# Kernel optimization log

Hardware: AMD Instinct MI355X
Metric: run time of the kernel (lower is better)

The kernel has to match this reference:

```python
import jax, jax.numpy as jnp
import numpy as np

D_MODEL = 1024
NUM_HEADS = 16
D_K = D_MODEL // NUM_HEADS


def setup_inputs() -> dict:
    key = jax.random.key(0)
    k1, k2, k3, k4 = jax.random.split(key, 4)
    x = jax.random.normal(k1, (2, 2048, D_MODEL), dtype=jnp.float32)
    # qkv_proj: Linear(d_model, 3*d_model, bias=False); stored as [in, out] for x @ W
    W_qkv = jax.random.normal(k2, (D_MODEL, 3 * D_MODEL), dtype=jnp.float32) * (1.0 / np.sqrt(D_MODEL))
    W_out = jax.random.normal(k3, (D_MODEL, D_MODEL), dtype=jnp.float32) * (1.0 / np.sqrt(D_MODEL))
    b_out = jax.random.normal(k4, (D_MODEL,), dtype=jnp.float32) * 0.01
    return {"x": x, "W_qkv": W_qkv, "W_out": W_out, "b_out": b_out}


def reference(x, W_qkv, W_out, b_out):
    B, N, C = x.shape
    scale = 1.0 / np.sqrt(D_K)
    qkv = (x @ W_qkv).reshape(B, N, 3, NUM_HEADS, D_K)
    qkv = jnp.transpose(qkv, (2, 0, 3, 1, 4))  # [3, B, H, N, d_k]
    q, k, v = qkv[0], qkv[1], qkv[2]
    scores = jnp.einsum("bhqd,bhkd->bhqk", q, k) * scale  # [B,H,N,N]
    attn = jax.nn.softmax(scores, axis=-1)
    out = jnp.einsum("bhqk,bhkd->bhqd", attn, v)  # [B,H,N,d_k]
    out = jnp.transpose(out, (0, 2, 1, 3)).reshape(B, N, C)
    return out @ W_out + b_out
```

## Files before the change

### kernel.cpp

```cpp
#include <hip/hip_runtime.h>
#include <cstdint>

typedef __bf16 bf16_t;
typedef __bf16 bf16x8 __attribute__((ext_vector_type(8)));
typedef float  f32x4  __attribute__((ext_vector_type(4)));
typedef uint32_t u32x4 __attribute__((ext_vector_type(4)));

#define MFMA16(a,b,c) __builtin_amdgcn_mfma_f32_16x16x32_bf16((a),(b),(c),0,0,0)

__device__ __forceinline__ void gload_lds16(const bf16_t* g, bf16_t* l) {
  __builtin_amdgcn_global_load_lds(
      (const __attribute__((address_space(1))) unsigned int*)g,
      (__attribute__((address_space(3))) unsigned int*)l,
      16, 0, 0);
}

__device__ __forceinline__ uint32_t cvt_pk_bf16(float lo, float hi) {
  uint32_t r;
  asm("v_cvt_pk_bf16_f32 %0, %1, %2" : "=v"(r) : "v"(lo), "v"(hi));
  return r;
}

__global__ void k_conv_x(const float* __restrict__ x, bf16_t* __restrict__ xb) {
  int i = blockIdx.x * blockDim.x + threadIdx.x;
  const float4* p = reinterpret_cast<const float4*>(x) + (size_t)i * 2;
  float4 a = p[0], b = p[1];
  bf16x8 v;
  v[0]=(bf16_t)a.x; v[1]=(bf16_t)a.y; v[2]=(bf16_t)a.z; v[3]=(bf16_t)a.w;
  v[4]=(bf16_t)b.x; v[5]=(bf16_t)b.y; v[6]=(bf16_t)b.z; v[7]=(bf16_t)b.w;
  *reinterpret_cast<bf16x8*>(xb + (size_t)i * 8) = v;
}

__global__ void k_transpose_w(const float* __restrict__ W, bf16_t* __restrict__ WT,
                              int K, int N) {
  __shared__ float tile[32][33];
  int n0 = blockIdx.x * 32, k0 = blockIdx.y * 32;
  int c = threadIdx.x & 31, r8 = threadIdx.x >> 5;
#pragma unroll
  for (int rr = 0; rr < 4; rr++) {
    int r = r8 + rr * 8;
    tile[r][c] = W[(size_t)(k0 + r) * N + n0 + c];
  }
  __syncthreads();
#pragma unroll
  for (int rr = 0; rr < 4; rr++) {
    int r = r8 + rr * 8;
    WT[(size_t)(n0 + r) * K + k0 + c] = (bf16_t)tile[c][r];
  }
}

__global__ void k_vtrans(const bf16_t* __restrict__ V, bf16_t* __restrict__ VT) {
  __shared__ bf16_t t[64 * 72];
  int bi = blockIdx.x;
  int head = bi >> 5, kt = bi & 31;
  int tid = threadIdx.x;
  const bf16_t* src = V + (size_t)head * 131072 + (size_t)kt * 64 * 64;
#pragma unroll
  for (int j = 0; j < 2; j++) {
    int q = tid + 256 * j;
    int key = q >> 3, part = q & 7;
    bf16x8 v = *reinterpret_cast<const bf16x8*>(src + key * 64 + part * 8);
    *reinterpret_cast<bf16x8*>(&t[key * 72 + part * 8]) = v;
  }
  __syncthreads();
  bf16_t* dst = VT + (size_t)head * 131072 + kt * 64;
#pragma unroll
  for (int j = 0; j < 2; j++) {
    int q = tid + 256 * j;
    int dv = q >> 3, part = q & 7;
    bf16x8 v;
#pragma unroll
    for (int e = 0; e < 8; e++) v[e] = t[(part * 8 + e) * 72 + dv];
    *reinterpret_cast<bf16x8*>(dst + (size_t)dv * 2048 + part * 8) = v;
  }
}

template<int EPI, int MT>
__global__ __launch_bounds__(256, 2) void k_gemm(
    const bf16_t* __restrict__ A, const bf16_t* __restrict__ BT, int Klen,
    bf16_t* __restrict__ Qo, bf16_t* __restrict__ Ko, bf16_t* __restrict__ Vo,
    const float* __restrict__ bias, float* __restrict__ Out, int Nout) {
  constexpr int WM = MT / 2;
  constexpr int MF = WM / 16;
  __shared__ bf16_t As[2][MT * 32];
  __shared__ bf16_t Bs[2][4096];
  int tid = threadIdx.x, lane = tid & 63, wid = tid >> 6;
  int row0 = blockIdx.x * MT, col0 = blockIdx.y * 128;
  int wr = wid >> 1, wc = wid & 1;
  int g = lane >> 4, li = lane & 15;

  f32x4 acc[MF][4] = {};

  auto stage = [&](int buf, int kt) {
    int k0 = kt * 32;
#pragma unroll
    for (int j = 0; j < MT / 64; j++) {
      int q = tid + 256 * j;
      int r = q >> 2, part = q & 3;
      gload_lds16(A + (size_t)(row0 + r) * Klen + k0 + part * 8,
                  &As[buf][q * 8]);
    }
#pragma unroll
    for (int j = 0; j < 2; j++) {
      int q = tid + 256 * j;
      int r = q >> 2, part = q & 3;
      gload_lds16(BT + (size_t)(col0 + r) * Klen + k0 + part * 8,
                  &Bs[buf][q * 8]);
    }
  };

  int nk = Klen >> 5;
  stage(0, 0);
  for (int kt = 0; kt < nk; kt++) {
    __syncthreads();
    if (kt + 1 < nk) stage((kt + 1) & 1, kt + 1);
    int buf = kt & 1;
    int kl = g * 8;
    bf16x8 a[MF], b[4];
#pragma unroll
    for (int m = 0; m < MF; m++)
      a[m] = *reinterpret_cast<const bf16x8*>(&As[buf][(wr * WM + m * 16 + li) * 32 + kl]);
#pragma unroll
    for (int n = 0; n < 4; n++)
      b[n] = *reinterpret_cast<const bf16x8*>(&Bs[buf][(wc * 64 + n * 16 + li) * 32 + kl]);
#pragma unroll
    for (int m = 0; m < MF; m++)
#pragma unroll
      for (int n = 0; n < 4; n++)
        acc[m][n] = MFMA16(a[m], b[n], acc[m][n]);
  }

#pragma unroll
  for (int m = 0; m < MF; m++) {
    int rg = row0 + wr * WM + m * 16 + g * 4;
#pragma unroll
    for (int n = 0; n < 4; n++) {
      int cg = col0 + wc * 64 + n * 16 + li;
#pragma unroll
      for (int i = 0; i < 4; i++) {
        float v = acc[m][n][i];
        int row = rg + i;
        if constexpr (EPI == 0) {
          int t = cg >> 10, h = (cg >> 6) & 15, dk = cg & 63;
          int b2 = row >> 11, nn = row & 2047;
          size_t idx = ((size_t)((b2 << 4) + h) * 2048 + nn) * 64 + dk;
          if (t == 0)      Qo[idx] = (bf16_t)(v * 0.18033688011112042f);
          else if (t == 1) Ko[idx] = (bf16_t)v;
          else             Vo[idx] = (bf16_t)v;
        } else {
          Out[(size_t)row * Nout + cg] = v + bias[cg];
        }
      }
    }
  }
}

__global__ __launch_bounds__(256, 2) void k_flash(
    const bf16_t* __restrict__ Q, const bf16_t* __restrict__ K,
    const bf16_t* __restrict__ VT, bf16_t* __restrict__ O) {
  __shared__ bf16_t Ks[2][64 * 64];
  __shared__ bf16_t Vs[2][64 * 64];

  int bi = (blockIdx.x & 7) * 64 + (blockIdx.x >> 3);
  int head = bi >> 4, qt = bi & 15;
  int tid = threadIdx.x, lane = tid & 63, wid = tid >> 6;
  int g = lane >> 4, li = lane & 15;

  const bf16_t* Qh = Q + (size_t)head * 131072 + (size_t)qt * 128 * 64;
  const bf16_t* Kh = K + (size_t)head * 131072;
  const bf16_t* Vh = VT + (size_t)head * 131072;

  bf16x8 qf[2][2];
#pragma unroll
  for (int rg = 0; rg < 2; rg++) {
    const bf16_t* qrow = Qh + (size_t)(wid * 32 + rg * 16 + li) * 64;
    qf[rg][0] = *reinterpret_cast<const bf16x8*>(qrow + g * 8);
    qf[rg][1] = *reinterpret_cast<const bf16x8*>(qrow + 32 + g * 8);
  }

  u32x4 onesw;
  onesw[0] = 0x3F803F80u; onesw[1] = 0x3F803F80u;
  onesw[2] = 0x3F803F80u; onesw[3] = 0x3F803F80u;
  bf16x8 ones = __builtin_bit_cast(bf16x8, onesw);

  f32x4 o[2][4] = {};
  f32x4 osum[2] = {};
  float mrun[2] = {0.f, 0.f};

  auto stage = [&](int buf, int t) {
    int kv0 = t * 64;
#pragma unroll
    for (int j = 0; j < 2; j++) {
      int q = tid + 256 * j;
      int key = q >> 3, part = q & 7;
      int sw = (key & 7) ^ (((key >> 3) & 3) << 1);
      gload_lds16(Kh + (size_t)(kv0 + key) * 64 + ((part ^ sw) * 8),
                  &Ks[buf][(tid + j * 256) * 8]);
    }
#pragma unroll
    for (int j = 0; j < 2; j++) {
      int q = tid + 256 * j;
      int dv = q >> 3, part = q & 7;
      gload_lds16(Vh + (size_t)dv * 2048 + kv0 + ((part ^ (dv & 7)) * 8),
                  &Vs[buf][(tid + j * 256) * 8]);
    }
  };

  stage(0, 0);
  for (int t = 0; t < 32; t++) {
    __syncthreads();
    if (t + 1 < 32) stage((t + 1) & 1, t + 1);
    int buf = t & 1;
    char* KsB = (char*)&Ks[buf][0];
    char* VsB = (char*)&Vs[buf][0];

    bf16x8 ka[2][4];
#pragma unroll
    for (int kd = 0; kd < 2; kd++)
#pragma unroll
      for (int nf = 0; nf < 4; nf++) {
        int key = ((li >> 2) << 3) | ((nf & 1) << 2) | (li & 3) | ((nf >> 1) << 5);
        int sw = (key & 7) ^ (((key >> 3) & 3) << 1);
        ka[kd][nf] = *reinterpret_cast<const bf16x8*>(
            KsB + key * 128 + (((kd * 4 + g) ^ sw) << 4));
      }

    f32x4 s[2][4];
#pragma unroll
    for (int rg = 0; rg < 2; rg++) {
      float nm = -mrun[rg];
#pragma unroll
      for (int nf = 0; nf < 4; nf++) {
        s[rg][nf][0] = nm; s[rg][nf][1] = nm; s[rg][nf][2] = nm; s[rg][nf][3] = nm;
      }
    }
    __builtin_amdgcn_s_setprio(1);
#pragma unroll
    for (int kd = 0; kd < 2; kd++)
#pragma unroll
      for (int nf = 0; nf < 4; nf++) {
        s[0][nf] = MFMA16(ka[kd][nf], qf[0][kd], s[0][nf]);
        s[1][nf] = MFMA16(ka[kd][nf], qf[1][kd], s[1][nf]);
      }
    __builtin_amdgcn_s_setprio(0);

    float pmax[2];
#pragma unroll
    for (int rg = 0; rg < 2; rg++) {
      float t0 = fmaxf(fmaxf(s[rg][0][0], s[rg][0][1]), s[rg][0][2]);
      float t1 = fmaxf(fmaxf(s[rg][0][3], s[rg][1][0]), s[rg][1][1]);
      float t2 = fmaxf(fmaxf(s[rg][1][2], s[rg][1][3]), s[rg][2][0]);
      float t3 = fmaxf(fmaxf(s[rg][2][1], s[rg][2][2]), s[rg][2][3]);
      float t4 = fmaxf(fmaxf(s[rg][3][0], s[rg][3][1]), s[rg][3][2]);
      pmax[rg] = fmaxf(fmaxf(fmaxf(t0, t1), fmaxf(t2, t3)), fmaxf(t4, s[rg][3][3]));
    }

    bool ok = (pmax[0] <= 8.f) & (pmax[1] <= 8.f);
    if (!__all(ok)) {
#pragma unroll
      for (int rg = 0; rg < 2; rg++) {
        float v = pmax[rg];
        v = fmaxf(v, __shfl_xor(v, 16));
        v = fmaxf(v, __shfl_xor(v, 32));
        float d = fmaxf(v, 0.f);
        float sc = __builtin_amdgcn_exp2f(-d);
        mrun[rg] += d;
#pragma unroll
        for (int nf = 0; nf < 4; nf++)
#pragma unroll
          for (int i = 0; i < 4; i++) s[rg][nf][i] -= d;
        float osc[4];
#pragma unroll
        for (int i = 0; i < 4; i++) osc[i] = __shfl(sc, g * 4 + i);
#pragma unroll
        for (int nf = 0; nf < 4; nf++)
#pragma unroll
          for (int i = 0; i < 4; i++) o[rg][nf][i] *= osc[i];
#pragma unroll
        for (int i = 0; i < 4; i++) osum[rg][i] *= osc[i];
      }
    }

    bf16x8 pa[2][2];
#pragma unroll
    for (int rg = 0; rg < 2; rg++) {
#pragma unroll
      for (int nf = 0; nf < 4; nf++)
#pragma unroll
        for (int i = 0; i < 4; i++)
          s[rg][nf][i] = __builtin_amdgcn_exp2f(s[rg][nf][i]);
      u32x4 w0, w1;
      w0[0] = cvt_pk_bf16(s[rg][0][0], s[rg][0][1]);
      w0[1] = cvt_pk_bf16(s[rg][0][2], s[rg][0][3]);
      w0[2] = cvt_pk_bf16(s[rg][1][0], s[rg][1][1]);
      w0[3] = cvt_pk_bf16(s[rg][1][2], s[rg][1][3]);
      w1[0] = cvt_pk_bf16(s[rg][2][0], s[rg][2][1]);
      w1[1] = cvt_pk_bf16(s[rg][2][2], s[rg][2][3]);
      w1[2] = cvt_pk_bf16(s[rg][3][0], s[rg][3][1]);
      w1[3] = cvt_pk_bf16(s[rg][3][2], s[rg][3][3]);
      pa[rg][0] = __builtin_bit_cast(bf16x8, w0);
      pa[rg][1] = __builtin_bit_cast(bf16x8, w1);
    }

    __builtin_amdgcn_s_setprio(1);
    osum[0] = MFMA16(pa[0][0], ones, osum[0]);
    osum[0] = MFMA16(pa[0][1], ones, osum[0]);
    osum[1] = MFMA16(pa[1][0], ones, osum[1]);
    osum[1] = MFMA16(pa[1][1], ones, osum[1]);
#pragma unroll
    for (int nfv = 0; nfv < 4; nfv++) {
      int dv = nfv * 16 + li;
      bf16x8 b0 = *reinterpret_cast<const bf16x8*>(
          VsB + dv * 128 + ((g * 16) ^ ((dv & 7) << 4)));
      bf16x8 b1 = *reinterpret_cast<const bf16x8*>(
          VsB + dv * 128 + ((64 + g * 16) ^ ((dv & 7) << 4)));
      o[0][nfv] = MFMA16(pa[0][0], b0, o[0][nfv]);
      o[0][nfv] = MFMA16(pa[0][1], b1, o[0][nfv]);
      o[1][nfv] = MFMA16(pa[1][0], b0, o[1][nfv]);
      o[1][nfv] = MFMA16(pa[1][1], b1, o[1][nfv]);
    }
    __builtin_amdgcn_s_setprio(0);
  }

  int b2 = head >> 4, h = head & 15;
#pragma unroll
  for (int rg = 0; rg < 2; rg++) {
#pragma unroll
    for (int i = 0; i < 4; i++) {
      float inv = 1.f / osum[rg][i];
      int n = qt * 128 + wid * 32 + rg * 16 + g * 4 + i;
      size_t base = ((size_t)b2 * 2048 + n) * 1024 + h * 64;
#pragma unroll
      for (int nfv = 0; nfv < 4; nfv++)
        O[base + nfv * 16 + li] = (bf16_t)(o[rg][nfv][i] * inv);
    }
  }
}

extern "C" void kernel_launch(void* const* d_in, const int* in_sizes, int n_in,
                              void* d_out, int out_size, void* d_ws, size_t ws_size,
                              hipStream_t stream) {
  const float* x    = (const float*)d_in[0];
  const float* Wqkv = (const float*)d_in[1];
  const float* Wout = (const float*)d_in[2];
  const float* bout = (const float*)d_in[3];
  float* out = (float*)d_out;

  char* ws = (char*)d_ws;
  bf16_t* xb    = (bf16_t*)(ws);
  bf16_t* wqkvT = (bf16_t*)(ws + ((size_t)8  << 20));
  bf16_t* woutT = (bf16_t*)(ws + ((size_t)14 << 20));
  bf16_t* qw    = (bf16_t*)(ws + ((size_t)16 << 20));
  bf16_t* kw    = (bf16_t*)(ws + ((size_t)24 << 20));
  bf16_t* vw    = (bf16_t*)(ws + ((size_t)32 << 20));
  bf16_t* vtw   = (bf16_t*)(ws + ((size_t)40 << 20));
  bf16_t* ow    = (bf16_t*)(ws + ((size_t)48 << 20));

  k_conv_x<<<2048, 256, 0, stream>>>(x, xb);
  k_transpose_w<<<dim3(96, 32), 256, 0, stream>>>(Wqkv, wqkvT, 1024, 3072);
  k_transpose_w<<<dim3(32, 32), 256, 0, stream>>>(Wout, woutT, 1024, 1024);
  k_gemm<0,128><<<dim3(32, 24), 256, 0, stream>>>(xb, wqkvT, 1024, qw, kw, vw,
                                                  nullptr, nullptr, 0);
  k_vtrans<<<1024, 256, 0, stream>>>(vw, vtw);
  k_flash<<<512, 256, 0, stream>>>(qw, kw, vtw, ow);
  k_gemm<1,64><<<dim3(64, 8), 256, 0, stream>>>(ow, woutT, 1024,
                                                nullptr, nullptr, nullptr,
                                                bout, out, 1024);
}
```

Measured before the change: 118.9 us.

## Replace QKV projection GEMM with 256x256-tile, 8-wave pipelined kernel

```diff
diff --git a/kernel.cpp b/kernel.cpp
--- a/kernel.cpp
+++ b/kernel.cpp
@@ -73,6 +73,131 @@
     for (int e = 0; e < 8; e++) v[e] = t[(part * 8 + e) * 72 + dv];
     *reinterpret_cast<bf16x8*>(dst + (size_t)dv * 2048 + part * 8) = v;
   }
+}
+
+#define BAR()    __builtin_amdgcn_s_barrier()
+#define LGKM0()  do { asm volatile("s_waitcnt lgkmcnt(0)" ::: "memory"); \
+                      __builtin_amdgcn_sched_barrier(0); } while (0)
+#define VMW(n)   asm volatile("s_waitcnt vmcnt(" #n ")" ::: "memory")
+
+#define LDA(buf, mh) do {                                                   \
+    char* base_ = L + ((buf) * 2 + wr) * 16384;                             \
+    _Pragma("unroll")                                                       \
+    for (int mf = 0; mf < 4; mf++) {                                        \
+      int r_ = ((mh) * 64 + mf * 16 + li) * 128;                            \
+      a[mf][0] = *reinterpret_cast<const bf16x8*>(base_ + r_ + aoff0);      \
+      a[mf][1] = *reinterpret_cast<const bf16x8*>(base_ + r_ + aoff1);      \
+    } } while (0)
+
+#define LDB(buf, nh) do {                                                   \
+    char* base_ = L + 65536 + ((buf) * 2 + (wc >> 1)) * 16384;              \
+    _Pragma("unroll")                                                       \
+    for (int nf = 0; nf < 2; nf++) {                                        \
+      int r_ = (((wc & 1) * 64) + (nh) * 32 + nf * 16 + li) * 128;          \
+      b[nh][nf][0] = *reinterpret_cast<const bf16x8*>(base_ + r_ + aoff0);  \
+      b[nh][nf][1] = *reinterpret_cast<const bf16x8*>(base_ + r_ + aoff1);  \
+    } } while (0)
+
+#define QUAD(mh, nh) do {                                                   \
+    __builtin_amdgcn_s_setprio(1);                                          \
+    _Pragma("unroll")                                                       \
+    for (int mf = 0; mf < 4; mf++)                                          \
+      _Pragma("unroll")                                                     \
+      for (int nf = 0; nf < 2; nf++) {                                      \
+        acc[mh][nh][mf][nf] = MFMA16(a[mf][0], b[nh][nf][0], acc[mh][nh][mf][nf]); \
+        acc[mh][nh][mf][nf] = MFMA16(a[mf][1], b[nh][nf][1], acc[mh][nh][mf][nf]); \
+      }                                                                      \
+    __builtin_amdgcn_s_setprio(0); } while (0)
+
+__global__ __launch_bounds__(512, 2) void k_gemm_qkv(
+    const bf16_t* __restrict__ A, const bf16_t* __restrict__ BT, int Klen,
+    bf16_t* __restrict__ Qo, bf16_t* __restrict__ Ko, bf16_t* __restrict__ Vo) {
+  extern __shared__ bf16_t lds[];
+  int tid = threadIdx.x, lane = tid & 63, wid = tid >> 6;
+  int wr = wid >> 2, wc = wid & 3;
+  int g = lane >> 4, li = lane & 15;
+
+  int lin = (blockIdx.x & 7) * 24 + (blockIdx.x >> 3);
+  int bx = lin & 15, by = lin >> 4;
+  int row0 = bx * 256, col0 = by * 256;
+
+  char* L = (char*)lds;
+  int sw    = (li & 7) << 4;
+  int aoff0 = (g * 16) ^ sw;
+  int aoff1 = (g * 16 + 64) ^ sw;
+  int soff_e = ((((tid & 7) * 16) ^ (((tid >> 3) & 7) << 4))) >> 1;
+
+  f32x4 acc[2][2][4][2] = {};
+  bf16x8 a[4][2], b[2][2][2];
+
+  int nk = Klen >> 6;
+
+  auto stageA = [&](int h, int kt) {
+    int rb = row0 + h * 128 + (tid >> 3);
+    const bf16_t* src = A + (size_t)rb * Klen + kt * 64 + soff_e;
+    bf16_t* dst = lds + ((kt & 1) * 2 + h) * 8192 + tid * 8;
+    gload_lds16(src, dst);
+    gload_lds16(src + (size_t)64 * Klen, dst + 4096);
+  };
+  auto stageB = [&](int h, int kt) {
+    int rb = col0 + h * 128 + (tid >> 3);
+    const bf16_t* src = BT + (size_t)rb * Klen + kt * 64 + soff_e;
+    bf16_t* dst = lds + 32768 + ((kt & 1) * 2 + h) * 8192 + tid * 8;
+    gload_lds16(src, dst);
+    gload_lds16(src + (size_t)64 * Klen, dst + 4096);
+  };
+
+  stageA(0, 0); stageA(1, 0); stageB(0, 0); stageB(1, 0);
+  stageB(0, 1); stageB(1, 1);
+  VMW(4); BAR();
+
+  for (int i = 0; i < nk / 2; i++) {
+    int T1 = 2 * i + 1, T2 = 2 * i + 2, T3 = 2 * i + 3;
+    bool s2 = T2 < nk, s3 = T3 < nk;
+    LDA(0, 0); LDB(0, 0); stageA(0, T1);
+    BAR(); LGKM0(); QUAD(0, 0); BAR();
+    LDB(0, 1); stageA(1, T1);
+    BAR(); LGKM0(); QUAD(0, 1); BAR();
+    LDA(0, 1); if (s2) stageB(0, T2);
+    BAR(); LGKM0(); QUAD(1, 0); BAR();
+    if (s2) stageB(1, T2);
+    BAR(); QUAD(1, 1);
+    if (s2) { VMW(4); } else { VMW(0); }
+    BAR();
+    LDA(1, 0); LDB(1, 0); if (s2) stageA(0, T2);
+    BAR(); LGKM0(); QUAD(0, 0); BAR();
+    LDB(1, 1); if (s2) stageA(1, T2);
+    BAR(); LGKM0(); QUAD(0, 1); BAR();
+    LDA(1, 1); if (s3) stageB(0, T3);
+    BAR(); LGKM0(); QUAD(1, 0); BAR();
+    if (s3) stageB(1, T3);
+    BAR(); QUAD(1, 1);
+    if (s3) { VMW(4); } else { VMW(0); }
+    BAR();
+  }
+
+#pragma unroll
+  for (int mh = 0; mh < 2; mh++)
+#pragma unroll
+    for (int nh = 0; nh < 2; nh++)
+#pragma unroll
+      for (int mf = 0; mf < 4; mf++)
+#pragma unroll
+        for (int nf = 0; nf < 2; nf++) {
+          int rg = row0 + wr * 128 + mh * 64 + mf * 16 + g * 4;
+          int cg = col0 + wc * 64 + nh * 32 + nf * 16 + li;
+          int t = cg >> 10, h = (cg >> 6) & 15, dk = cg & 63;
+#pragma unroll
+          for (int ii = 0; ii < 4; ii++) {
+            float v = acc[mh][nh][mf][nf][ii];
+            int row = rg + ii;
+            int b2 = row >> 11, nn = row & 2047;
+            size_t idx = ((size_t)((b2 << 4) + h) * 2048 + nn) * 64 + dk;
+            if (t == 0)      Qo[idx] = (bf16_t)(v * 0.18033688011112042f);
+            else if (t == 1) Ko[idx] = (bf16_t)v;
+            else             Vo[idx] = (bf16_t)v;
+          }
+        }
 }
 
 template<int EPI, int MT>
@@ -356,11 +481,17 @@
   bf16_t* vtw   = (bf16_t*)(ws + ((size_t)40 << 20));
   bf16_t* ow    = (bf16_t*)(ws + ((size_t)48 << 20));
 
+  static bool attr_set = false;
+  if (!attr_set) {
+    hipFuncSetAttribute((const void*)k_gemm_qkv,
+                        hipFuncAttributeMaxDynamicSharedMemorySize, 131072);
+    attr_set = true;
+  }
+
   k_conv_x<<<2048, 256, 0, stream>>>(x, xb);
   k_transpose_w<<<dim3(96, 32), 256, 0, stream>>>(Wqkv, wqkvT, 1024, 3072);
   k_transpose_w<<<dim3(32, 32), 256, 0, stream>>>(Wout, woutT, 1024, 1024);
-  k_gemm<0,128><<<dim3(32, 24), 256, 0, stream>>>(xb, wqkvT, 1024, qw, kw, vw,
-                                                  nullptr, nullptr, 0);
+  k_gemm_qkv<<<192, 512, 131072, stream>>>(xb, wqkvT, 1024, qw, kw, vw);
   k_vtrans<<<1024, 256, 0, stream>>>(vw, vtw);
   k_flash<<<512, 256, 0, stream>>>(qw, kw, vtw, ow);
   k_gemm<1,64><<<dim3(64, 8), 256, 0, stream>>>(ow, woutT, 1024,
```

Result: no change. 117.6 us (-1.1%).
